# Kernel optimization log

Hardware: AMD Instinct MI355X
Metric: run time of the kernel (lower is better)

The kernel has to match this reference:

```python
import jax, jax.numpy as jnp
import numpy as np

K, A, DIM = 1024, 16384, 512


def setup_inputs() -> dict:
    key = jax.random.key(0)
    ks = jax.random.split(key, 8)
    B, H, W = 2048, 8, 8
    z_t = jax.random.randint(ks[0], (B, H, W), 0, K, dtype=jnp.int64)
    z_tp1 = jax.random.randint(ks[1], (B, H, W), 0, K, dtype=jnp.int64)
    embed_w = jax.random.normal(ks[2], (K, DIM), dtype=jnp.float32) * 0.02
    # MLP: Linear(2*dim -> dim), GELU, Linear(dim -> dim)
    lim1 = 1.0 / np.sqrt(2 * DIM)
    w1 = jax.random.uniform(ks[3], (2 * DIM, DIM), minval=-lim1, maxval=lim1, dtype=jnp.float32)
    b1 = jax.random.uniform(ks[4], (DIM,), minval=-lim1, maxval=lim1, dtype=jnp.float32)
    lim2 = 1.0 / np.sqrt(DIM)
    w2 = jax.random.uniform(ks[5], (DIM, DIM), minval=-lim2, maxval=lim2, dtype=jnp.float32)
    b2 = jax.random.uniform(ks[6], (DIM,), minval=-lim2, maxval=lim2, dtype=jnp.float32)
    codebook_w = jax.random.normal(ks[7], (A, DIM), dtype=jnp.float32) * 0.02
    return {"z_t": z_t, "z_tp1": z_tp1, "embed_w": embed_w, "w1": w1, "b1": b1,
            "w2": w2, "b2": b2, "codebook_w": codebook_w}


def reference(z_t, z_tp1, embed_w, w1, b1, w2, b2, codebook_w):
    B = z_t.shape[0]
    # embed int code grids and mean-pool over H*W tokens -> [B, dim]
    e_t = embed_w[z_t.reshape(B, -1)].mean(axis=1)
    e_tp1 = embed_w[z_tp1.reshape(B, -1)].mean(axis=1)
    h = jnp.concatenate([e_t, e_tp1], axis=-1)          # [B, 2*dim]
    h = jax.nn.gelu(h @ w1 + b1, approximate=False)
    e = h @ w2 + b2                                      # [B, dim]
    # VQ: squared L2 distance to each code, argmin, gather
    d2 = (jnp.sum(e * e, axis=1, keepdims=True)
          - 2.0 * e @ codebook_w.T
          + jnp.sum(codebook_w * codebook_w, axis=1)[None, :])  # [B, A]
    ids = jnp.argmin(d2, axis=1)                         # [B]
    q = codebook_w[ids]                                  # [B, dim]
    return ids, q
```

## Files before the change

kernel.cpp:

```cpp
#include <hip/hip_runtime.h>
#include <hip/hip_bf16.h>

#define TOK 64
#define DIMC 512

typedef __attribute__((ext_vector_type(8))) short v8s;
typedef __attribute__((ext_vector_type(4))) float v4f;

__device__ __forceinline__ unsigned int f2ord(float f) {
  unsigned int u = __float_as_uint(f);
  return (u & 0x80000000u) ? ~u : (u | 0x80000000u);
}

__device__ __forceinline__ float gelu_exact(float x) {
  return 0.5f * x * (1.0f + erff(x * 0.70710678118654752440f));
}

__device__ __forceinline__ unsigned short f2bf(float x) {
  unsigned int u = __float_as_uint(x);
  return (unsigned short)((u + 0x7FFFu + ((u >> 16) & 1u)) >> 16);
}
__device__ __forceinline__ float bf2f(unsigned short h) {
  return __uint_as_float((unsigned int)h << 16);
}

__device__ __forceinline__ void gl2lds16(const void* g, void* l) {
  __builtin_amdgcn_global_load_lds((const __attribute__((address_space(1))) void*)g,
                                   (__attribute__((address_space(3))) void*)l,
                                   16, 0, 0);
}

__global__ __launch_bounds__(256) void k_prep(
    const int* __restrict__ zt, const int* __restrict__ ztp,
    const float* __restrict__ emb,
    unsigned short* __restrict__ hh, unsigned short* __restrict__ hl,
    unsigned long long* __restrict__ rowmin,
    const float* __restrict__ w1, unsigned short* __restrict__ w1th,
    unsigned short* __restrict__ w1tl,
    const float* __restrict__ w2, unsigned short* __restrict__ w2th,
    unsigned short* __restrict__ w2tl,
    const float* __restrict__ cb, unsigned short* __restrict__ ch,
    unsigned short* __restrict__ cl, float* __restrict__ cnorm) {
  __shared__ int codes[128];
  __shared__ float tbuf[32][33];
  const int bid = blockIdx.x;
  const int tid = threadIdx.x;

  if (bid < 2048) {
    const int b = bid;
    if (tid < 64) codes[tid] = zt[b * TOK + tid];
    else if (tid < 128) codes[tid] = ztp[b * TOK + (tid - 64)];
    if (tid == 0) rowmin[b] = 0xFFFFFFFFFFFFFFFFull;
    __syncthreads();
    const int half = tid >> 7;
    const int c4 = tid & 127;
    const float4* emb4 = (const float4*)emb;
    float4 s = make_float4(0.f, 0.f, 0.f, 0.f);
    #pragma unroll 8
    for (int t = 0; t < TOK; t++) {
      const int code = codes[half * TOK + t];
      const float4 v = emb4[code * 128 + c4];
      s.x += v.x; s.y += v.y; s.z += v.z; s.w += v.w;
    }
    const float inv = 1.0f / 64.0f;
    float f[4] = {s.x * inv, s.y * inv, s.z * inv, s.w * inv};
    unsigned short hi[4], lo[4];
    #pragma unroll
    for (int i = 0; i < 4; i++) {
      hi[i] = f2bf(f[i]);
      lo[i] = f2bf(f[i] - bf2f(hi[i]));
    }
    const int off = b * 1024 + half * 512 + c4 * 4;
    *(ushort4*)&hh[off] = make_ushort4(hi[0], hi[1], hi[2], hi[3]);
    *(ushort4*)&hl[off] = make_ushort4(lo[0], lo[1], lo[2], lo[3]);
  } else if (bid < 2816) {
    const float* w; unsigned short *wth, *wtl; int Kd, N, k0, n0;
    if (bid < 2560) {
      const int i = bid - 2048;
      w = w1; wth = w1th; wtl = w1tl; Kd = 1024; N = 512;
      k0 = (i & 31) * 32; n0 = (i >> 5) * 32;
    } else {
      const int i = bid - 2560;
      w = w2; wth = w2th; wtl = w2tl; Kd = 512; N = 512;
      k0 = (i & 15) * 32; n0 = (i >> 4) * 32;
    }
    const int c = tid & 31, r = tid >> 5;
    #pragma unroll
    for (int i = 0; i < 4; i++)
      tbuf[r + i * 8][c] = w[(size_t)(k0 + r + i * 8) * N + n0 + c];
    __syncthreads();
    #pragma unroll
    for (int i = 0; i < 4; i++) {
      const float v = tbuf[c][r + i * 8];
      const unsigned short hi = f2bf(v);
      const unsigned short lo = f2bf(v - bf2f(hi));
      wth[(size_t)(n0 + r + i * 8) * Kd + k0 + c] = hi;
      wtl[(size_t)(n0 + r + i * 8) * Kd + k0 + c] = lo;
    }
  } else {
    const int row = (bid - 2816) * 4 + (tid >> 6);
    const int lane = tid & 63;
    const float4* cb4 = (const float4*)cb;
    const float4 va = cb4[row * 128 + lane * 2];
    const float4 vb = cb4[row * 128 + lane * 2 + 1];
    float s = va.x * va.x + va.y * va.y + va.z * va.z + va.w * va.w
            + vb.x * vb.x + vb.y * vb.y + vb.z * vb.z + vb.w * vb.w;
    float f[8] = {va.x, va.y, va.z, va.w, vb.x, vb.y, vb.z, vb.w};
    unsigned short hi[8], lo[8];
    #pragma unroll
    for (int i = 0; i < 8; i++) {
      hi[i] = f2bf(f[i]);
      lo[i] = f2bf(f[i] - bf2f(hi[i]));
    }
    ushort4* chp = (ushort4*)&ch[row * DIMC + lane * 8];
    ushort4* clp = (ushort4*)&cl[row * DIMC + lane * 8];
    chp[0] = make_ushort4(hi[0], hi[1], hi[2], hi[3]);
    chp[1] = make_ushort4(hi[4], hi[5], hi[6], hi[7]);
    clp[0] = make_ushort4(lo[0], lo[1], lo[2], lo[3]);
    clp[1] = make_ushort4(lo[4], lo[5], lo[6], lo[7]);
    #pragma unroll
    for (int off = 32; off > 0; off >>= 1) s += __shfl_down(s, off);
    if (lane == 0) cnorm[row] = s;
  }
}

template <bool GELU>
__global__ __launch_bounds__(256) void k_gemm(const unsigned short* __restrict__ Ah_,
                                              const unsigned short* __restrict__ Al_,
                                              const unsigned short* __restrict__ Bh_,
                                              const unsigned short* __restrict__ Bl_,
                                              const float* __restrict__ bias,
                                              unsigned short* __restrict__ oh,
                                              unsigned short* __restrict__ ol,
                                              int Kd, int N) {
  __shared__ unsigned short Ahs[64 * 32];
  __shared__ unsigned short Als[64 * 32];
  __shared__ unsigned short Bhs[64 * 32];
  __shared__ unsigned short Bls[64 * 32];

  const int tid = threadIdx.x;
  const int lane = tid & 63;
  const int wid = tid >> 6;
  const int m0 = blockIdx.x * 64;
  const int n0 = blockIdx.y * 64;

  v4f acc[2][2];
  #pragma unroll
  for (int i = 0; i < 2; i++)
    #pragma unroll
    for (int j = 0; j < 2; j++) acc[i][j] = (v4f)(0.f);

  const unsigned short* gsrc;
  unsigned short* ldst;
  if (wid == 0)      { gsrc = Ah_ + (size_t)m0 * Kd; ldst = Ahs; }
  else if (wid == 1) { gsrc = Al_ + (size_t)m0 * Kd; ldst = Als; }
  else if (wid == 2) { gsrc = Bh_ + (size_t)n0 * Kd; ldst = Bhs; }
  else               { gsrc = Bl_ + (size_t)n0 * Kd; ldst = Bls; }

  const int srow = lane >> 2;
  const int sk = (lane & 3) * 8;
  const int wm = wid >> 1, wn = wid & 1;
  const int fr = lane & 15;
  const int fq = (lane >> 4) * 8;

  for (int k0 = 0; k0 < Kd; k0 += 32) {
    __syncthreads();
    #pragma unroll
    for (int j = 0; j < 4; j++)
      gl2lds16(gsrc + (size_t)(j * 16 + srow) * Kd + k0 + sk, ldst + j * 512);
    __syncthreads();

    v8s ah[2], al[2], bh[2], bl[2];
    #pragma unroll
    for (int t = 0; t < 2; t++) {
      const int ar = (wm * 32 + t * 16 + fr) * 32 + fq;
      const int br = (wn * 32 + t * 16 + fr) * 32 + fq;
      ah[t] = *(const v8s*)&Ahs[ar];
      al[t] = *(const v8s*)&Als[ar];
      bh[t] = *(const v8s*)&Bhs[br];
      bl[t] = *(const v8s*)&Bls[br];
    }
    #pragma unroll
    for (int mt = 0; mt < 2; mt++)
      #pragma unroll
      for (int nt = 0; nt < 2; nt++) {
        acc[mt][nt] = __builtin_amdgcn_mfma_f32_16x16x32_bf16(ah[mt], bh[nt], acc[mt][nt], 0, 0, 0);
        acc[mt][nt] = __builtin_amdgcn_mfma_f32_16x16x32_bf16(ah[mt], bl[nt], acc[mt][nt], 0, 0, 0);
        acc[mt][nt] = __builtin_amdgcn_mfma_f32_16x16x32_bf16(al[mt], bh[nt], acc[mt][nt], 0, 0, 0);
      }
  }

  const int col16 = lane & 15;
  const int q = lane >> 4;
  int colv[2]; float bv[2];
  #pragma unroll
  for (int nt = 0; nt < 2; nt++) {
    colv[nt] = n0 + wn * 32 + nt * 16 + col16;
    bv[nt] = bias[colv[nt]];
  }
  #pragma unroll
  for (int mt = 0; mt < 2; mt++)
    #pragma unroll
    for (int reg = 0; reg < 4; reg++) {
      const int row = m0 + wm * 32 + mt * 16 + q * 4 + reg;
      #pragma unroll
      for (int nt = 0; nt < 2; nt++) {
        float v = acc[mt][nt][reg] + bv[nt];
        if (GELU) v = gelu_exact(v);
        const unsigned short hi = f2bf(v);
        oh[(size_t)row * N + colv[nt]] = hi;
        ol[(size_t)row * N + colv[nt]] = f2bf(v - bf2f(hi));
      }
    }
}

__global__ __launch_bounds__(256, 2) void k_vq(const unsigned short* __restrict__ eh,
                                               const unsigned short* __restrict__ el,
                                               const unsigned short* __restrict__ ch,
                                               const unsigned short* __restrict__ cl,
                                               const float* __restrict__ cnorm,
                                               unsigned long long* __restrict__ rowmin) {
  __shared__ unsigned short Ah[128 * 32];
  __shared__ unsigned short Al[128 * 32];
  __shared__ unsigned short Bh[256 * 32];
  __shared__ unsigned short Bl[256 * 32];

  const int tid = threadIdx.x;
  const int lane = tid & 63;
  const int wid = tid >> 6;
  const int bid = blockIdx.x;
  const int j = bid >> 3;
  const int x = j & 15;
  const int y = ((j >> 4) << 3) | (bid & 7);
  const int r0 = x * 128;
  const int c0 = y * 256;

  v4f acc[4][8];
  #pragma unroll
  for (int i = 0; i < 4; i++)
    #pragma unroll
    for (int jj = 0; jj < 8; jj++) acc[i][jj] = (v4f)(0.f);

  const unsigned short* ehB = eh + (size_t)r0 * DIMC;
  const unsigned short* elB = el + (size_t)r0 * DIMC;
  const unsigned short* chB = ch + (size_t)c0 * DIMC;
  const unsigned short* clB = cl + (size_t)c0 * DIMC;

  const int srow = lane >> 2;
  const int sk = (lane & 3) * 8;
  const int wm = wid >> 1;
  const int wn = wid & 1;
  const int fr = lane & 15;
  const int fq = (lane >> 4) * 8;

  for (int k0 = 0; k0 < DIMC; k0 += 32) {
    __syncthreads();
    #pragma unroll
    for (int u = 0; u < 12; u++) {
      const int i = wid * 12 + u;
      const unsigned short* gs; unsigned short* ls; int rbase;
      if (i < 8)       { gs = ehB; ls = Ah; rbase = i * 16; }
      else if (i < 16) { gs = elB; ls = Al; rbase = (i - 8) * 16; }
      else if (i < 32) { gs = chB; ls = Bh; rbase = (i - 16) * 16; }
      else             { gs = clB; ls = Bl; rbase = (i - 32) * 16; }
      gl2lds16(gs + (size_t)(rbase + srow) * DIMC + k0 + sk, ls + rbase * 32);
    }
    __syncthreads();

    v8s ahf[4], alf[4];
    #pragma unroll
    for (int mt = 0; mt < 4; mt++) {
      const int ar = (wm * 64 + mt * 16 + fr) * 32 + fq;
      ahf[mt] = *(const v8s*)&Ah[ar];
      alf[mt] = *(const v8s*)&Al[ar];
    }
    #pragma unroll
    for (int nt = 0; nt < 8; nt++) {
      const int br = (wn * 128 + nt * 16 + fr) * 32 + fq;
      const v8s bhf = *(const v8s*)&Bh[br];
      const v8s blf = *(const v8s*)&Bl[br];
      #pragma unroll
      for (int mt = 0; mt < 4; mt++) {
        acc[mt][nt] = __builtin_amdgcn_mfma_f32_16x16x32_bf16(ahf[mt], bhf, acc[mt][nt], 0, 0, 0);
        acc[mt][nt] = __builtin_amdgcn_mfma_f32_16x16x32_bf16(ahf[mt], blf, acc[mt][nt], 0, 0, 0);
        acc[mt][nt] = __builtin_amdgcn_mfma_f32_16x16x32_bf16(alf[mt], bhf, acc[mt][nt], 0, 0, 0);
      }
    }
  }

  const int col16 = lane & 15;
  const int q = lane >> 4;
  float cn[8];
  #pragma unroll
  for (int nt = 0; nt < 8; nt++) cn[nt] = cnorm[c0 + wn * 128 + nt * 16 + col16];

  #pragma unroll
  for (int mt = 0; mt < 4; mt++) {
    #pragma unroll
    for (int reg = 0; reg < 4; reg++) {
      const int row = r0 + wm * 64 + mt * 16 + q * 4 + reg;
      float best = fmaf(-2.f, acc[mt][0][reg], cn[0]);
      int bid2 = c0 + wn * 128 + col16;
      #pragma unroll
      for (int nt = 1; nt < 8; nt++) {
        const float s = fmaf(-2.f, acc[mt][nt][reg], cn[nt]);
        const int id = c0 + wn * 128 + nt * 16 + col16;
        if (s < best) { best = s; bid2 = id; }
      }
      unsigned long long v =
          ((unsigned long long)f2ord(best) << 32) | (unsigned int)bid2;
      #pragma unroll
      for (int off = 8; off > 0; off >>= 1) {
        const unsigned long long o = __shfl_down(v, off, 16);
        if (o < v) v = o;
      }
      if (col16 == 0) atomicMin(&rowmin[row], v);
    }
  }
}

__global__ __launch_bounds__(64) void k_final(const unsigned long long* __restrict__ rowmin,
                                              const float* __restrict__ cb,
                                              float* __restrict__ out,
                                              int B) {
  const int b = blockIdx.x;
  const int t = threadIdx.x;
  const unsigned long long m = rowmin[b];
  const int id = (int)(unsigned int)(m & 0xFFFFFFFFull);
  if (t == 0) out[b] = (float)id;
  float4* q4 = (float4*)(out + B) + b * 128;
  const float4* cb4 = (const float4*)cb + (size_t)id * 128;
  q4[t] = cb4[t];
  q4[t + 64] = cb4[t + 64];
}

extern "C" void kernel_launch(void* const* d_in, const int* in_sizes, int n_in,
                              void* d_out, int out_size, void* d_ws, size_t ws_size,
                              hipStream_t stream) {
  const int* zt = (const int*)d_in[0];
  const int* ztp = (const int*)d_in[1];
  const float* emb = (const float*)d_in[2];
  const float* w1 = (const float*)d_in[3];
  const float* b1 = (const float*)d_in[4];
  const float* w2 = (const float*)d_in[5];
  const float* b2 = (const float*)d_in[6];
  const float* cb = (const float*)d_in[7];
  float* out = (float*)d_out;

  const int B = in_sizes[0] / TOK;
  const int A = in_sizes[7] / DIMC;

  char* p = (char*)d_ws;
  unsigned short* hh = (unsigned short*)p;  p += (size_t)B * 1024 * 2;
  unsigned short* hl = (unsigned short*)p;  p += (size_t)B * 1024 * 2;
  unsigned short* w1th = (unsigned short*)p; p += (size_t)512 * 1024 * 2;
  unsigned short* w1tl = (unsigned short*)p; p += (size_t)512 * 1024 * 2;
  unsigned short* w2th = (unsigned short*)p; p += (size_t)512 * 512 * 2;
  unsigned short* w2tl = (unsigned short*)p; p += (size_t)512 * 512 * 2;
  unsigned short* h1h = (unsigned short*)p; p += (size_t)B * DIMC * 2;
  unsigned short* h1l = (unsigned short*)p; p += (size_t)B * DIMC * 2;
  unsigned short* eh = (unsigned short*)p;  p += (size_t)B * DIMC * 2;
  unsigned short* el = (unsigned short*)p;  p += (size_t)B * DIMC * 2;
  unsigned short* ch = (unsigned short*)p;  p += (size_t)A * DIMC * 2;
  unsigned short* cl = (unsigned short*)p;  p += (size_t)A * DIMC * 2;
  float* cnorm = (float*)p;                 p += (size_t)A * 4;
  unsigned long long* rowmin = (unsigned long long*)p;

  k_prep<<<2816 + A / 4, 256, 0, stream>>>(zt, ztp, emb, hh, hl, rowmin,
                                           w1, w1th, w1tl, w2, w2th, w2tl,
                                           cb, ch, cl, cnorm);
  k_gemm<true><<<dim3(B / 64, 512 / 64), 256, 0, stream>>>(hh, hl, w1th, w1tl, b1, h1h, h1l, 1024, 512);
  k_gemm<false><<<dim3(B / 64, 512 / 64), 256, 0, stream>>>(h1h, h1l, w2th, w2tl, b2, eh, el, 512, 512);
  k_vq<<<(B / 128) * (A / 256), 256, 0, stream>>>(eh, el, ch, cl, cnorm, rowmin);
  k_final<<<B, 64, 0, stream>>>(rowmin, cb, out, B);
}
```

Before: 235.4 us.

## Double-buffer MLP GEMM LDS tiles, shrink M tile to 32, raise VQ occupancy

```diff
diff --git a/kernel.cpp b/kernel.cpp
--- a/kernel.cpp
+++ b/kernel.cpp
@@ -133,29 +133,21 @@
                                               unsigned short* __restrict__ oh,
                                               unsigned short* __restrict__ ol,
                                               int Kd, int N) {
-  __shared__ unsigned short Ahs[64 * 32];
-  __shared__ unsigned short Als[64 * 32];
-  __shared__ unsigned short Bhs[64 * 32];
-  __shared__ unsigned short Bls[64 * 32];
+  __shared__ unsigned short AhS[2][32 * 32];
+  __shared__ unsigned short AlS[2][32 * 32];
+  __shared__ unsigned short BhS[2][64 * 32];
+  __shared__ unsigned short BlS[2][64 * 32];
 
   const int tid = threadIdx.x;
   const int lane = tid & 63;
   const int wid = tid >> 6;
-  const int m0 = blockIdx.x * 64;
+  const int m0 = blockIdx.x * 32;
   const int n0 = blockIdx.y * 64;
 
-  v4f acc[2][2];
-  #pragma unroll
-  for (int i = 0; i < 2; i++)
-    #pragma unroll
-    for (int j = 0; j < 2; j++) acc[i][j] = (v4f)(0.f);
-
-  const unsigned short* gsrc;
-  unsigned short* ldst;
-  if (wid == 0)      { gsrc = Ah_ + (size_t)m0 * Kd; ldst = Ahs; }
-  else if (wid == 1) { gsrc = Al_ + (size_t)m0 * Kd; ldst = Als; }
-  else if (wid == 2) { gsrc = Bh_ + (size_t)n0 * Kd; ldst = Bhs; }
-  else               { gsrc = Bl_ + (size_t)n0 * Kd; ldst = Bls; }
+  const unsigned short* Ab_h = Ah_ + (size_t)m0 * Kd;
+  const unsigned short* Ab_l = Al_ + (size_t)m0 * Kd;
+  const unsigned short* Bb_h = Bh_ + (size_t)n0 * Kd;
+  const unsigned short* Bb_l = Bl_ + (size_t)n0 * Kd;
 
   const int srow = lane >> 2;
   const int sk = (lane & 3) * 8;
@@ -163,58 +155,63 @@
   const int fr = lane & 15;
   const int fq = (lane >> 4) * 8;
 
+  v4f acc[2];
+  acc[0] = (v4f)(0.f);
+  acc[1] = (v4f)(0.f);
+
+  auto stage = [&](int b, int k0) {
+    #pragma unroll
+    for (int u = 0; u < 3; u++) {
+      const int i = wid * 3 + u;
+      const unsigned short* gs; unsigned short* ls; int rbase;
+      if (i < 2)      { gs = Ab_h; ls = AhS[b]; rbase = i * 16; }
+      else if (i < 4) { gs = Ab_l; ls = AlS[b]; rbase = (i - 2) * 16; }
+      else if (i < 8) { gs = Bb_h; ls = BhS[b]; rbase = (i - 4) * 16; }
+      else            { gs = Bb_l; ls = BlS[b]; rbase = (i - 8) * 16; }
+      gl2lds16(gs + (size_t)(rbase + srow) * Kd + k0 + sk, ls + rbase * 32);
+    }
+  };
+
+  stage(0, 0);
+  int cur = 0;
   for (int k0 = 0; k0 < Kd; k0 += 32) {
     __syncthreads();
-    #pragma unroll
-    for (int j = 0; j < 4; j++)
-      gl2lds16(gsrc + (size_t)(j * 16 + srow) * Kd + k0 + sk, ldst + j * 512);
-    __syncthreads();
-
-    v8s ah[2], al[2], bh[2], bl[2];
-    #pragma unroll
-    for (int t = 0; t < 2; t++) {
-      const int ar = (wm * 32 + t * 16 + fr) * 32 + fq;
-      const int br = (wn * 32 + t * 16 + fr) * 32 + fq;
-      ah[t] = *(const v8s*)&Ahs[ar];
-      al[t] = *(const v8s*)&Als[ar];
-      bh[t] = *(const v8s*)&Bhs[br];
-      bl[t] = *(const v8s*)&Bls[br];
-    }
-    #pragma unroll
-    for (int mt = 0; mt < 2; mt++)
-      #pragma unroll
-      for (int nt = 0; nt < 2; nt++) {
-        acc[mt][nt] = __builtin_amdgcn_mfma_f32_16x16x32_bf16(ah[mt], bh[nt], acc[mt][nt], 0, 0, 0);
-        acc[mt][nt] = __builtin_amdgcn_mfma_f32_16x16x32_bf16(ah[mt], bl[nt], acc[mt][nt], 0, 0, 0);
-        acc[mt][nt] = __builtin_amdgcn_mfma_f32_16x16x32_bf16(al[mt], bh[nt], acc[mt][nt], 0, 0, 0);
-      }
+    if (k0 + 32 < Kd) stage(cur ^ 1, k0 + 32);
+
+    const int ar = (wm * 16 + fr) * 32 + fq;
+    const v8s ah = *(const v8s*)&AhS[cur][ar];
+    const v8s al = *(const v8s*)&AlS[cur][ar];
+    #pragma unroll
+    for (int nt = 0; nt < 2; nt++) {
+      const int br = (wn * 32 + nt * 16 + fr) * 32 + fq;
+      const v8s bh = *(const v8s*)&BhS[cur][br];
+      const v8s bl = *(const v8s*)&BlS[cur][br];
+      acc[nt] = __builtin_amdgcn_mfma_f32_16x16x32_bf16(ah, bh, acc[nt], 0, 0, 0);
+      acc[nt] = __builtin_amdgcn_mfma_f32_16x16x32_bf16(ah, bl, acc[nt], 0, 0, 0);
+      acc[nt] = __builtin_amdgcn_mfma_f32_16x16x32_bf16(al, bh, acc[nt], 0, 0, 0);
+    }
+    cur ^= 1;
   }
 
   const int col16 = lane & 15;
   const int q = lane >> 4;
-  int colv[2]; float bv[2];
   #pragma unroll
   for (int nt = 0; nt < 2; nt++) {
-    colv[nt] = n0 + wn * 32 + nt * 16 + col16;
-    bv[nt] = bias[colv[nt]];
-  }
-  #pragma unroll
-  for (int mt = 0; mt < 2; mt++)
+    const int col = n0 + wn * 32 + nt * 16 + col16;
+    const float bv = bias[col];
     #pragma unroll
     for (int reg = 0; reg < 4; reg++) {
-      const int row = m0 + wm * 32 + mt * 16 + q * 4 + reg;
-      #pragma unroll
-      for (int nt = 0; nt < 2; nt++) {
-        float v = acc[mt][nt][reg] + bv[nt];
-        if (GELU) v = gelu_exact(v);
-        const unsigned short hi = f2bf(v);
-        oh[(size_t)row * N + colv[nt]] = hi;
-        ol[(size_t)row * N + colv[nt]] = f2bf(v - bf2f(hi));
-      }
-    }
-}
-
-__global__ __launch_bounds__(256, 2) void k_vq(const unsigned short* __restrict__ eh,
+      const int row = m0 + wm * 16 + q * 4 + reg;
+      float v = acc[nt][reg] + bv;
+      if (GELU) v = gelu_exact(v);
+      const unsigned short hi = f2bf(v);
+      oh[(size_t)row * N + col] = hi;
+      ol[(size_t)row * N + col] = f2bf(v - bf2f(hi));
+    }
+  }
+}
+
+__global__ __launch_bounds__(256, 3) void k_vq(const unsigned short* __restrict__ eh,
                                                const unsigned short* __restrict__ el,
                                                const unsigned short* __restrict__ ch,
                                                const unsigned short* __restrict__ cl,
@@ -369,8 +366,8 @@
   k_prep<<<2816 + A / 4, 256, 0, stream>>>(zt, ztp, emb, hh, hl, rowmin,
                                            w1, w1th, w1tl, w2, w2th, w2tl,
                                            cb, ch, cl, cnorm);
-  k_gemm<true><<<dim3(B / 64, 512 / 64), 256, 0, stream>>>(hh, hl, w1th, w1tl, b1, h1h, h1l, 1024, 512);
-  k_gemm<false><<<dim3(B / 64, 512 / 64), 256, 0, stream>>>(h1h, h1l, w2th, w2tl, b2, eh, el, 512, 512);
+  k_gemm<true><<<dim3(B / 32, 512 / 64), 256, 0, stream>>>(hh, hl, w1th, w1tl, b1, h1h, h1l, 1024, 512);
+  k_gemm<false><<<dim3(B / 32, 512 / 64), 256, 0, stream>>>(h1h, h1l, w2th, w2tl, b2, eh, el, 512, 512);
   k_vq<<<(B / 128) * (A / 256), 256, 0, stream>>>(eh, el, ch, cl, cnorm, rowmin);
   k_final<<<B, 64, 0, stream>>>(rowmin, cb, out, B);
 }
```

Result: slower. 436.8 us (+85.6%).
